# Kernel optimization log

Measured on AMD Instinct MI355X. Metric: run time of the kernel, lower is better.

## Reference

```python
import jax, jax.numpy as jnp
import numpy as np

B, T = 64, 64
HUMAN, IN = 64, 8
HS, ES, K = 1024, 1024, 7
PSI_H, PSI_LR = 1024, 30

_PAR_SHAPES = [(HS, HS), (HS,), (IN, HS), (HS, HUMAN), (IN, HUMAN - IN)]
_PAR_SIZES = [int(np.prod(s)) for s in _PAR_SHAPES]
N_PSI = int(sum(_PAR_SIZES))
_OFFS = np.cumsum([0] + _PAR_SIZES)


def setup_inputs() -> dict:
    key = jax.random.key(0)
    ks = jax.random.split(key, 16)
    def xav(k, shape):
        lim = float(np.sqrt(6.0 / (shape[0] + shape[1])))
        return jax.random.uniform(k, shape, minval=-lim, maxval=lim, dtype=jnp.float32)
    def uni(k, shape, s):
        return jax.random.uniform(k, shape, minval=-s, maxval=s, dtype=jnp.float32)
    se = float(1.0 / np.sqrt(ES))
    return {
        "inputs": jax.random.normal(ks[0], (B, T, IN), jnp.float32),
        "outputs": jax.random.normal(ks[1], (B, T, HUMAN), jnp.float32),
        "eps": jax.random.normal(ks[2], (B, K), jnp.float32),
        "enc_Wih": uni(ks[3], (3 * ES, HUMAN), se),
        "enc_Whh": uni(ks[4], (3 * ES, ES), se),
        "enc_bih": uni(ks[5], (3 * ES,), se),
        "enc_bhh": uni(ks[6], (3 * ES,), se),
        "to_mu": xav(ks[7], (ES, K)),
        "to_lsigma": xav(ks[8], (ES, K)),
        "to_lsigma_bias": -0.5 * jnp.ones((K,), jnp.float32),
        "W1": xav(ks[9], (K, PSI_H)),
        "b1": jnp.zeros((PSI_H,), jnp.float32),
        "W2": xav(ks[10], (PSI_H, PSI_LR)),
        "b2": jnp.zeros((PSI_LR,), jnp.float32),
        "W3": xav(ks[11], (PSI_LR, N_PSI)),
        "b3": jnp.zeros((N_PSI,), jnp.float32),
        "gru_Wih": xav(ks[12], (IN, 2 * HS)),
        "gru_Whh": xav(ks[13], (HS, 2 * HS)),
        "gru_bias": jnp.concatenate([jnp.zeros((HS,)), jnp.ones((HS,))]).astype(jnp.float32),
    }


def _gru_cell(h, x, Wih, Whh, bih, bhh):
    # torch.nn.GRUCell math, gate order (r, z, n)
    gx = x @ Wih.T + bih
    gh = h @ Whh.T + bhh
    xr, xz, xn = jnp.split(gx, 3, axis=-1)
    hr, hz, hn = jnp.split(gh, 3, axis=-1)
    r = jax.nn.sigmoid(xr + hr)
    z = jax.nn.sigmoid(xz + hz)
    n = jnp.tanh(xn + r * hn)
    return (1.0 - z) * n + z * h


def _split_psi(psi):
    # psi: [B, N_PSI] -> per-sample (Whh, bh, Wih, C, D)
    return [psi[:, _OFFS[i]:_OFFS[i + 1]].reshape((-1,) + _PAR_SHAPES[i]) for i in range(5)]


def reference(inputs, outputs, eps, enc_Wih, enc_Whh, enc_bih, enc_bhh,
              to_mu, to_lsigma, to_lsigma_bias, W1, b1, W2, b2, W3, b3,
              gru_Wih, gru_Whh, gru_bias):
    bsz = inputs.shape[0]
    # ---- encoder: GRUCell over time-major outputs ----
    out_tm = jnp.swapaxes(outputs, 0, 1)  # [T, B, HUMAN]
    h0 = jnp.zeros((bsz, ES), inputs.dtype)
    h_enc = _gru_cell(h0, out_tm[0], enc_Wih, enc_Whh, enc_bih, enc_bhh)
    def enc_step(h, x):
        h = _gru_cell(h, x, enc_Wih, enc_Whh, enc_bih, enc_bhh)
        return h, None
    h_enc, _ = jax.lax.scan(enc_step, h_enc, out_tm[1:])
    mu = h_enc @ to_mu                       # [B, K]
    logstd = h_enc @ to_lsigma + to_lsigma_bias
    z = mu + eps * jnp.exp(logstd)
    # ---- hypernetwork psi decoder ----
    psi = (jnp.tanh(z @ W1 + b1) @ W2 + b2) @ W3 + b3   # [B, N_PSI]
    Whh_b, bh_b, Wih_b, C_b, D_b = _split_psi(psi)
    # ---- per-sample GRU decoder, vectorized over batch, scan over time ----
    gx_all = jnp.einsum('bti,ij->tbj', inputs, gru_Wih)  # [T, B, 2*HS]
    xW_all = jnp.einsum('bti,bih->tbh', inputs, Wih_b)   # [T, B, HS]

    def dec_step(h, xs):
        gx_t, xW_t = xs
        pre = gx_t + h @ gru_Whh + gru_bias   # [B, 2*HS]
        z_t = jax.nn.sigmoid(pre[:, :HS])
        r_t = jax.nn.sigmoid(pre[:, HS:])
        hWhh = jnp.einsum('bh,bhk->bk', h, Whh_b) + bh_b
        eta = jnp.tanh(xW_t + r_t * jnp.tanh(hWhh))
        h_new = z_t * h + (1.0 - z_t) * eta
        return h_new, h_new

    state0 = jnp.zeros((bsz, HS), inputs.dtype)
    h_last, dec_seq = jax.lax.scan(dec_step, state0, (gx_all, xW_all))
    dec_seq = jnp.swapaxes(dec_seq, 0, 1)    # [B, T, HS]
    # ---- readout ----
    yhats = jnp.einsum('bth,bhm->btm', dec_seq, C_b)
    xD = jnp.einsum('bti,bim->btm', inputs, D_b)  # [B, T, HUMAN-IN]
    yhats = yhats + jnp.concatenate([jnp.zeros_like(inputs), xD], axis=-1)
    # residual output
    yhats = yhats + jnp.concatenate(
        [inputs, jnp.zeros((bsz, inputs.shape[1], HUMAN - IN), inputs.dtype)], axis=-1)
    states = jax.lax.stop_gradient(h_last)
    return yhats, mu, logstd, states
```

## Files before the change

### kernel.cpp

```cpp
#include <hip/hip_runtime.h>

namespace {
constexpr int nT = 64;
constexpr int nK = 7;
constexpr long N_PSI = 1123776;
constexpr long SZ_WHH = 1048576;
constexpr long REST_SZ = 75200;
constexpr long R_BH = 0;
constexpr long R_WIH = 1024;
constexpr long R_C = 9216;
constexpr long R_D = 74752;
constexpr int NCH = 16;
constexpr long PHALF = (long)NCH * 64 * 1024;
}

typedef __attribute__((ext_vector_type(4))) unsigned short us4;

__device__ __forceinline__ float b2f(unsigned short u) {
  return __uint_as_float(((unsigned int)u) << 16);
}
__device__ __forceinline__ unsigned short f2b(float f) {
  unsigned int u = __float_as_uint(f);
  return (unsigned short)((u + 0x7fffu + ((u >> 16) & 1u)) >> 16);
}
__device__ __forceinline__ float sigm(float x) { return 1.f / (1.f + __expf(-x)); }

__global__ void transpose_bf16_k(const float* __restrict__ in, unsigned short* __restrict__ out,
                                 int rows, int cols) {
  __shared__ float tile[32][33];
  int x = blockIdx.x * 32 + threadIdx.x;
  int y = blockIdx.y * 32 + threadIdx.y;
  #pragma unroll
  for (int i = 0; i < 32; i += 8)
    if ((y + i) < rows && x < cols) tile[threadIdx.y + i][threadIdx.x] = in[(long)(y + i) * cols + x];
  __syncthreads();
  x = blockIdx.y * 32 + threadIdx.x;
  y = blockIdx.x * 32 + threadIdx.y;
  #pragma unroll
  for (int i = 0; i < 32; i += 8)
    if ((y + i) < cols && x < rows) out[(long)(y + i) * rows + x] = f2b(tile[threadIdx.x][threadIdx.y + i]);
}

__global__ void cvt_bf16_k(const float* __restrict__ in, unsigned short* __restrict__ out, long n) {
  long i = (long)blockIdx.x * 256 + threadIdx.x;
  if (i < n) out[i] = f2b(in[i]);
}

__global__ __launch_bounds__(256) void enc_gx_k(const float* __restrict__ outputs,
                                                const unsigned short* __restrict__ WtWihB,
                                                const float* __restrict__ bih,
                                                unsigned short* __restrict__ gxE) {
  int g0 = blockIdx.x * 256;
  int btg = blockIdx.y;
  __shared__ unsigned short ws[64 * 256];
  __shared__ float xs[64][64];
  for (int i = threadIdx.x; i < 64 * 256; i += 256)
    ws[i] = WtWihB[(long)(i >> 8) * 3072 + g0 + (i & 255)];
  for (int i = threadIdx.x; i < 64 * 64; i += 256) {
    int idx = btg * 64 + (i >> 6);
    int t = idx >> 6, b = idx & 63;
    xs[i >> 6][i & 63] = outputs[((long)b * nT + t) * 64 + (i & 63)];
  }
  __syncthreads();
  float bihv = bih[g0 + threadIdx.x];
  for (int j = 0; j < 64; ++j) {
    int idx = btg * 64 + j;
    float acc = bihv;
    #pragma unroll 8
    for (int i = 0; i < 64; ++i) acc += xs[j][i] * b2f(ws[i * 256 + threadIdx.x]);
    gxE[(long)idx * 3072 + g0 + threadIdx.x] = f2b(acc);
  }
}

__global__ __launch_bounds__(256) void dec_gx_k(const float* __restrict__ inputs,
                                                const float* __restrict__ gWih,
                                                const float* __restrict__ gbias,
                                                unsigned short* __restrict__ gxD) {
  int g0 = blockIdx.x * 256;
  int btg = blockIdx.y;
  __shared__ float ws[8][256];
  __shared__ float xs[64][8];
  for (int i = threadIdx.x; i < 8 * 256; i += 256)
    ws[i >> 8][i & 255] = gWih[(long)(i >> 8) * 2048 + g0 + (i & 255)];
  for (int i = threadIdx.x; i < 64 * 8; i += 256) {
    int idx = btg * 64 + (i >> 3);
    int t = idx >> 6, b = idx & 63;
    xs[i >> 3][i & 7] = inputs[((long)b * nT + t) * 8 + (i & 7)];
  }
  __syncthreads();
  float bv = gbias[g0 + threadIdx.x];
  for (int j = 0; j < 64; ++j) {
    int idx = btg * 64 + j;
    float acc = bv;
    #pragma unroll
    for (int i = 0; i < 8; ++i) acc += xs[j][i] * ws[i][threadIdx.x];
    gxD[(long)idx * 2048 + g0 + threadIdx.x] = f2b(acc);
  }
}

__global__ __launch_bounds__(256) void xW_k(const float* __restrict__ inputs,
                                            const float* __restrict__ Rest,
                                            unsigned short* __restrict__ xWb) {
  int k0 = blockIdx.x * 256;
  int b = blockIdx.y;
  __shared__ float ws[8][256];
  __shared__ float xs[64][8];
  const float* RB = Rest + (long)b * REST_SZ + R_WIH;
  for (int i = threadIdx.x; i < 8 * 256; i += 256)
    ws[i >> 8][i & 255] = RB[(long)(i >> 8) * 1024 + k0 + (i & 255)];
  for (int i = threadIdx.x; i < 64 * 8; i += 256)
    xs[i >> 3][i & 7] = inputs[((long)b * nT + (i >> 3)) * 8 + (i & 7)];
  __syncthreads();
  for (int t = 0; t < 64; ++t) {
    float acc = 0.f;
    #pragma unroll
    for (int i = 0; i < 8; ++i) acc += xs[t][i] * ws[i][threadIdx.x];
    xWb[((long)t * 64 + b) * 1024 + k0 + threadIdx.x] = f2b(acc);
  }
}

__global__ __launch_bounds__(512, 2) void enc_step3_k(
    const unsigned short* __restrict__ W,
    const unsigned short* __restrict__ gxE,
    const float* __restrict__ bhh,
    float* __restrict__ hEnc,
    const float* __restrict__ pRr, const float* __restrict__ pZr, const float* __restrict__ pNr,
    float* __restrict__ pRw, float* __restrict__ pZw, float* __restrict__ pNw,
    int t) {
  int c = blockIdx.x & (NCH - 1);
  int sp = blockIdx.x >> 4;
  int b0 = sp * 2, b1 = b0 + 1;
  __shared__ float h0s[64], h1s[64];
  __shared__ float red[3][4][128];
  int v = threadIdx.x;
  {
    int q = v >> 7, idx = v & 127;
    int bb = (idx >> 6) ? b1 : b0;
    int e = c * 64 + (idx & 63);
    float sr = 0.f, sz = 0.f, sn = 0.f;
    if (t > 0) {
      #pragma unroll
      for (int cc = q * 4; cc < q * 4 + 4; ++cc) {
        long base = ((long)cc * 64 + bb) * 1024 + e;
        sr += pRr[base]; sz += pZr[base]; sn += pNr[base];
      }
    }
    red[0][q][idx] = sr; red[1][q][idx] = sz; red[2][q][idx] = sn;
  }
  __syncthreads();
  if (v < 128) {
    int hi = v >> 6;
    int bb = hi ? b1 : b0;
    int e = c * 64 + (v & 63);
    float sr = red[0][0][v] + red[0][1][v] + red[0][2][v] + red[0][3][v];
    float sz = red[1][0][v] + red[1][1][v] + red[1][2][v] + red[1][3][v];
    float sn = red[2][0][v] + red[2][1][v] + red[2][2][v] + red[2][3][v];
    long gb = ((long)t * 64 + bb) * 3072;
    float xr = b2f(gxE[gb + e]), xz = b2f(gxE[gb + 1024 + e]), xn = b2f(gxE[gb + 2048 + e]);
    float hr = sr + bhh[e], hz = sz + bhh[1024 + e], hn = sn + bhh[2048 + e];
    float r = sigm(xr + hr);
    float z = sigm(xz + hz);
    float n = tanhf(xn + r * hn);
    float hold = (t > 0) ? hEnc[(long)bb * 1024 + e] : 0.f;
    float hnew = (1.f - z) * n + z * hold;
    hEnc[(long)bb * 1024 + e] = hnew;
    if (hi) h1s[v & 63] = hnew; else h0s[v & 63] = hnew;
  }
  __syncthreads();
  if (t < nT - 1) {
    if (v < 256) {
      int e0 = v * 4;
      float ar0[4] = {}, az0[4] = {}, ar1[4] = {}, az1[4] = {};
      const unsigned short* Wb = W + (long)(c * 64) * 3072 + e0;
      #pragma unroll 4
      for (int j = 0; j < 64; ++j) {
        us4 wr = *(const us4*)(Wb + (long)j * 3072);
        us4 wz = *(const us4*)(Wb + (long)j * 3072 + 1024);
        float hv0 = h0s[j], hv1 = h1s[j];
        #pragma unroll
        for (int q = 0; q < 4; ++q) {
          float fr = b2f(wr[q]), fz = b2f(wz[q]);
          ar0[q] += hv0 * fr; az0[q] += hv0 * fz;
          ar1[q] += hv1 * fr; az1[q] += hv1 * fz;
        }
      }
      long i0 = ((long)c * 64 + b0) * 1024 + e0;
      long i1 = i0 + 1024;
      *(float4*)(pRw + i0) = make_float4(ar0[0], ar0[1], ar0[2], ar0[3]);
      *(float4*)(pZw + i0) = make_float4(az0[0], az0[1], az0[2], az0[3]);
      *(float4*)(pRw + i1) = make_float4(ar1[0], ar1[1], ar1[2], ar1[3]);
      *(float4*)(pZw + i1) = make_float4(az1[0], az1[1], az1[2], az1[3]);
    } else {
      int e0 = (v - 256) * 4;
      float an0[4] = {}, an1[4] = {};
      const unsigned short* Wb = W + (long)(c * 64) * 3072 + 2048 + e0;
      #pragma unroll 8
      for (int j = 0; j < 64; ++j) {
        us4 wn = *(const us4*)(Wb + (long)j * 3072);
        float hv0 = h0s[j], hv1 = h1s[j];
        #pragma unroll
        for (int q = 0; q < 4; ++q) {
          float fn = b2f(wn[q]);
          an0[q] += hv0 * fn; an1[q] += hv1 * fn;
        }
      }
      long i0 = ((long)c * 64 + b0) * 1024 + e0;
      long i1 = i0 + 1024;
      *(float4*)(pNw + i0) = make_float4(an0[0], an0[1], an0[2], an0[3]);
      *(float4*)(pNw + i1) = make_float4(an1[0], an1[1], an1[2], an1[3]);
    }
  }
}

__global__ __launch_bounds__(256) void latent_hyper_k(
    const float* __restrict__ h_enc,
    const float* __restrict__ to_mu, const float* __restrict__ to_lsig,
    const float* __restrict__ lsig_bias, const float* __restrict__ eps,
    const float* __restrict__ W1, const float* __restrict__ b1,
    const float* __restrict__ W2, const float* __restrict__ b2,
    float* __restrict__ out_mu, float* __restrict__ out_lsig,
    float* __restrict__ a2out) {
  int b = blockIdx.x;
  __shared__ float hs[1024];
  __shared__ float zv[8];
  __shared__ float a1[1024];
  for (int i = threadIdx.x; i < 1024; i += 256) hs[i] = h_enc[b * 1024 + i];
  __syncthreads();
  int g = threadIdx.x >> 5, s = threadIdx.x & 31;
  if (g < nK) {
    float am = 0.f, as_ = 0.f;
    for (int h = s; h < 1024; h += 32) {
      float hv = hs[h];
      am += hv * to_mu[h * nK + g];
      as_ += hv * to_lsig[h * nK + g];
    }
    #pragma unroll
    for (int m = 16; m >= 1; m >>= 1) { am += __shfl_xor(am, m); as_ += __shfl_xor(as_, m); }
    if (s == 0) {
      float ls = as_ + lsig_bias[g];
      out_mu[b * nK + g] = am;
      out_lsig[b * nK + g] = ls;
      zv[g] = am + eps[b * nK + g] * __expf(ls);
    }
  }
  __syncthreads();
  for (int j = threadIdx.x; j < 1024; j += 256) {
    float acc = b1[j];
    #pragma unroll
    for (int i = 0; i < nK; ++i) acc += zv[i] * W1[i * 1024 + j];
    a1[j] = tanhf(acc);
  }
  __syncthreads();
  int l = threadIdx.x >> 3, s8 = threadIdx.x & 7;
  if (l < 30) {
    float acc = 0.f;
    for (int j = s8; j < 1024; j += 8) acc += a1[j] * W2[j * 30 + l];
    acc += __shfl_xor(acc, 4);
    acc += __shfl_xor(acc, 2);
    acc += __shfl_xor(acc, 1);
    if (s8 == 0) a2out[b * 30 + l] = acc + b2[l];
  }
}

__global__ __launch_bounds__(256) void psi_q8_k(
    const float* __restrict__ a2, const float* __restrict__ W3, const float* __restrict__ b3,
    char* __restrict__ Q8, float* __restrict__ sdec ) {
  __shared__ float sa[64 * 30];
  for (int i = threadIdx.x; i < 64 * 30; i += 256) sa[i] = a2[i];
  int h = blockIdx.x >> 1, half = blockIdx.x & 1;
  int wv = threadIdx.x >> 6, lane = threadIdx.x & 63;
  int g = half * 4 + wv;
  long n0 = (long)h * 1024 + g * 128 + lane * 2;
  float2 w[30];
  #pragma unroll
  for (int l = 0; l < 30; ++l) w[l] = *(const float2*)(W3 + (long)l * N_PSI + n0);
  float2 bb = *(const float2*)(b3 + n0);
  __syncthreads();
  for (int b = 0; b < 64; ++b) {
    float a0 = bb.x, a1 = bb.y;
    const float* ab = &sa[b * 30];
    #pragma unroll
    for (int l = 0; l < 30; ++l) { float av = ab[l]; a0 += av * w[l].x; a1 += av * w[l].y; }
    float m = fmaxf(fabsf(a0), fabsf(a1));
    #pragma unroll
    for (int d = 32; d >= 1; d >>= 1) m = fmaxf(m, __shfl_xor(m, d));
    float inv = (m > 0.f) ? 127.f / m : 0.f;
    int q0 = __float2int_rn(a0 * inv);
    int q1 = __float2int_rn(a1 * inv);
    q0 = min(127, max(-127, q0));
    q1 = min(127, max(-127, q1));
    *(char2*)(Q8 + (long)b * SZ_WHH + n0) = make_char2((char)q0, (char)q1);
    if (lane == 0) sdec[((long)b * 1024 + h) * 8 + g] = m * (1.f / 127.f);
  }
}

__global__ __launch_bounds__(256) void psi_rest_k(
    const float* __restrict__ a2, const float* __restrict__ W3, const float* __restrict__ b3,
    float* __restrict__ Rest) {
  __shared__ float sa[64 * 30];
  for (int i = threadIdx.x; i < 64 * 30; i += 256) sa[i] = a2[i];
  long n0 = SZ_WHH + ((long)blockIdx.x * 256 + threadIdx.x) * 2;
  __syncthreads();
  if (n0 >= N_PSI) return;
  float2 w[30];
  #pragma unroll
  for (int l = 0; l < 30; ++l) w[l] = *(const float2*)(W3 + (long)l * N_PSI + n0);
  float2 bb = *(const float2*)(b3 + n0);
  long r = n0 - SZ_WHH;
  for (int b = 0; b < 64; ++b) {
    float a0 = bb.x, a1 = bb.y;
    const float* ab = &sa[b * 30];
    #pragma unroll
    for (int l = 0; l < 30; ++l) { float av = ab[l]; a0 += av * w[l].x; a1 += av * w[l].y; }
    *(float2*)(Rest + (long)b * REST_SZ + r) = make_float2(a0, a1);
  }
}

__global__ __launch_bounds__(512, 2) void dec_step_q8g_k(
    const char* __restrict__ Q8,
    const float* __restrict__ sdec,
    const unsigned short* __restrict__ gWhhB,
    const unsigned short* __restrict__ gxD,
    const unsigned short* __restrict__ xWb,
    const float* __restrict__ Rest,
    float* __restrict__ decS,
    const float* __restrict__ pZr, const float* __restrict__ pRr, const float* __restrict__ pWr,
    float* __restrict__ pZw, float* __restrict__ pRw, float* __restrict__ pWw,
    int t) {
  int c = blockIdx.x & (NCH - 1);
  int sp = blockIdx.x >> 4;
  int b0 = sp * 2, b1 = b0 + 1;
  __shared__ float h0s[64], h1s[64];
  __shared__ float h0q[8][64], h1q[8][64];
  __shared__ float red[3][4][128];
  int v = threadIdx.x;
  {
    int q = v >> 7, idx = v & 127;
    int bb = (idx >> 6) ? b1 : b0;
    int k = c * 64 + (idx & 63);
    float sz = 0.f, sr = 0.f, sw = 0.f;
    if (t > 0) {
      #pragma unroll
      for (int cc = q * 4; cc < q * 4 + 4; ++cc) {
        long base = ((long)cc * 64 + bb) * 1024 + k;
        sz += pZr[base]; sr += pRr[base]; sw += pWr[base];
      }
    }
    red[0][q][idx] = sz; red[1][q][idx] = sr; red[2][q][idx] = sw;
  }
  __syncthreads();
  if (v < 128) {
    int hi = v >> 6;
    int bb = hi ? b1 : b0;
    int k = c * 64 + (v & 63);
    float sz = red[0][0][v] + red[0][1][v] + red[0][2][v] + red[0][3][v];
    float sr = red[1][0][v] + red[1][1][v] + red[1][2][v] + red[1][3][v];
    float sw = red[2][0][v] + red[2][1][v] + red[2][2][v] + red[2][3][v];
    long gb = ((long)t * 64 + bb) * 2048;
    float gz = b2f(gxD[gb + k]), gr = b2f(gxD[gb + 1024 + k]);
    float z = sigm(gz + sz);
    float r = sigm(gr + sr);
    float hW = sw + Rest[(long)bb * REST_SZ + R_BH + k];
    float xw = b2f(xWb[((long)t * 64 + bb) * 1024 + k]);
    float eta = tanhf(xw + r * tanhf(hW));
    float hold = (t > 0) ? decS[((long)bb * nT + (t - 1)) * 1024 + k] : 0.f;
    float hnew = z * hold + (1.f - z) * eta;
    decS[((long)bb * nT + t) * 1024 + k] = hnew;
    const float* sc = sdec + ((long)bb * 1024 + k) * 8;
    float4 scA = *(const float4*)(sc);
    float4 scB = *(const float4*)(sc + 4);
    int row = v & 63;
    if (hi) {
      h1s[row] = hnew;
      h1q[0][row] = hnew * scA.x; h1q[1][row] = hnew * scA.y;
      h1q[2][row] = hnew * scA.z; h1q[3][row] = hnew * scA.w;
      h1q[4][row] = hnew * scB.x; h1q[5][row] = hnew * scB.y;
      h1q[6][row] = hnew * scB.z; h1q[7][row] = hnew * scB.w;
    } else {
      h0s[row] = hnew;
      h0q[0][row] = hnew * scA.x; h0q[1][row] = hnew * scA.y;
      h0q[2][row] = hnew * scA.z; h0q[3][row] = hnew * scA.w;
      h0q[4][row] = hnew * scB.x; h0q[5][row] = hnew * scB.y;
      h0q[6][row] = hnew * scB.z; h0q[7][row] = hnew * scB.w;
    }
  }
  __syncthreads();
  if (t < nT - 1) {
    if (v < 256) {
      int k0 = v * 4;
      float az0[4] = {}, ar0[4] = {}, az1[4] = {}, ar1[4] = {};
      const unsigned short* G = gWhhB + (long)(c * 64) * 2048 + k0;
      #pragma unroll 4
      for (int j = 0; j < 64; ++j) {
        us4 wz = *(const us4*)(G + (long)j * 2048);
        us4 wr = *(const us4*)(G + (long)j * 2048 + 1024);
        float hv0 = h0s[j], hv1 = h1s[j];
        #pragma unroll
        for (int q = 0; q < 4; ++q) {
          float fz = b2f(wz[q]), fr = b2f(wr[q]);
          az0[q] += hv0 * fz; ar0[q] += hv0 * fr;
          az1[q] += hv1 * fz; ar1[q] += hv1 * fr;
        }
      }
      long i0 = ((long)c * 64 + b0) * 1024 + k0;
      long i1 = i0 + 1024;
      *(float4*)(pZw + i0) = make_float4(az0[0], az0[1], az0[2], az0[3]);
      *(float4*)(pRw + i0) = make_float4(ar0[0], ar0[1], ar0[2], ar0[3]);
      *(float4*)(pZw + i1) = make_float4(az1[0], az1[1], az1[2], az1[3]);
      *(float4*)(pRw + i1) = make_float4(ar1[0], ar1[1], ar1[2], ar1[3]);
    } else {
      int k0 = (v - 256) * 4;
      int g = k0 >> 7;
      const float* hq0 = h0q[g];
      const float* hq1 = h1q[g];
      float aw0[4] = {}, aw1[4] = {};
      const char* Q0 = Q8 + (long)b0 * SZ_WHH + (long)(c * 64) * 1024 + k0;
      const char* Q1 = Q8 + (long)b1 * SZ_WHH + (long)(c * 64) * 1024 + k0;
      #pragma unroll 8
      for (int j = 0; j < 64; ++j) {
        char4 q0 = *(const char4*)(Q0 + (long)j * 1024);
        char4 q1 = *(const char4*)(Q1 + (long)j * 1024);
        float hv0 = hq0[j], hv1 = hq1[j];
        aw0[0] += hv0 * (float)q0.x; aw0[1] += hv0 * (float)q0.y;
        aw0[2] += hv0 * (float)q0.z; aw0[3] += hv0 * (float)q0.w;
        aw1[0] += hv1 * (float)q1.x; aw1[1] += hv1 * (float)q1.y;
        aw1[2] += hv1 * (float)q1.z; aw1[3] += hv1 * (float)q1.w;
      }
      long i0 = ((long)c * 64 + b0) * 1024 + k0;
      long i1 = i0 + 1024;
      *(float4*)(pWw + i0) = make_float4(aw0[0], aw0[1], aw0[2], aw0[3]);
      *(float4*)(pWw + i1) = make_float4(aw1[0], aw1[1], aw1[2], aw1[3]);
    }
  }
}

__global__ __launch_bounds__(256) void readout_k(
    const float* __restrict__ dec_seq, const float* __restrict__ inputs,
    const float* __restrict__ Rest, float* __restrict__ yhats) {
  int b = blockIdx.x >> 3;
  int tg = blockIdx.x & 7;
  __shared__ float ss[8][1024];
  __shared__ float part[4][8][64];
  for (int i = threadIdx.x; i < 8 * 1024; i += 256)
    ss[i >> 10][i & 1023] = dec_seq[((long)b * nT + tg * 8 + (i >> 10)) * 1024 + (i & 1023)];
  __syncthreads();
  int m = threadIdx.x & 63, hq = threadIdx.x >> 6;
  const float* C = Rest + (long)b * REST_SZ + R_C;
  float acc[8] = {};
  for (int h = hq * 256; h < hq * 256 + 256; ++h) {
    float cv = C[(long)h * 64 + m];
    #pragma unroll
    for (int tt = 0; tt < 8; ++tt) acc[tt] += ss[tt][h] * cv;
  }
  #pragma unroll
  for (int tt = 0; tt < 8; ++tt) part[hq][tt][m] = acc[tt];
  __syncthreads();
  const float* D = Rest + (long)b * REST_SZ + R_D;
  for (int o = threadIdx.x; o < 512; o += 256) {
    int tt = o >> 6, mm = o & 63;
    float a = part[0][tt][mm] + part[1][tt][mm] + part[2][tt][mm] + part[3][tt][mm];
    long bt = (long)b * nT + tg * 8 + tt;
    if (mm < 8) {
      a += inputs[bt * 8 + mm];
    } else {
      #pragma unroll
      for (int i = 0; i < 8; ++i) a += inputs[bt * 8 + i] * D[i * 56 + (mm - 8)];
    }
    yhats[bt * 64 + mm] = a;
  }
}

__global__ void copy_states_k(const float* __restrict__ dec_seq, float* __restrict__ states) {
  int i = blockIdx.x * 256 + threadIdx.x;
  int b = i >> 10, h = i & 1023;
  states[i] = dec_seq[((long)b * nT + (nT - 1)) * 1024 + h];
}

extern "C" void kernel_launch(void* const* d_in, const int* in_sizes, int n_in,
                              void* d_out, int out_size, void* d_ws, size_t ws_size,
                              hipStream_t stream) {
  const float* inputs  = (const float*)d_in[0];
  const float* outputs = (const float*)d_in[1];
  const float* eps     = (const float*)d_in[2];
  const float* enc_Wih = (const float*)d_in[3];
  const float* enc_Whh = (const float*)d_in[4];
  const float* enc_bih = (const float*)d_in[5];
  const float* enc_bhh = (const float*)d_in[6];
  const float* to_mu   = (const float*)d_in[7];
  const float* to_lsig = (const float*)d_in[8];
  const float* lsig_b  = (const float*)d_in[9];
  const float* W1 = (const float*)d_in[10];
  const float* b1 = (const float*)d_in[11];
  const float* W2 = (const float*)d_in[12];
  const float* b2 = (const float*)d_in[13];
  const float* W3 = (const float*)d_in[14];
  const float* b3 = (const float*)d_in[15];
  const float* gWih  = (const float*)d_in[16];
  const float* gWhh  = (const float*)d_in[17];
  const float* gbias = (const float*)d_in[18];

  char* ws = (char*)d_ws;
  size_t off = 0;
  auto alloc = [&](size_t bytes) { size_t o = off; off = (off + bytes + 255) & ~(size_t)255; return o; };
  size_t oRest   = alloc(64ull * REST_SZ * 4);
  size_t oQ8     = alloc(64ull * SZ_WHH);
  size_t oSdec   = alloc(64ull * 1024 * 8 * 4);
  size_t ogWhhB  = alloc(1024ull * 2048 * 2);
  size_t oWtWhhB = alloc(1024ull * 3072 * 2);
  size_t oWtWihB = alloc(64ull * 3072 * 2);
  size_t ogxE    = alloc(64ull * 64 * 3072 * 2);
  size_t ogxD    = alloc(64ull * 64 * 2048 * 2);
  size_t oxWb    = alloc(64ull * 64 * 1024 * 2);
  size_t opA     = alloc((size_t)2 * PHALF * 4);
  size_t opB     = alloc((size_t)2 * PHALF * 4);
  size_t opC     = alloc((size_t)2 * PHALF * 4);
  size_t ohA     = alloc(64ull * 1024 * 4);
  size_t oDec    = alloc(64ull * 64 * 1024 * 4);
  size_t oA2     = alloc(64 * 30 * 4);
  (void)in_sizes; (void)n_in; (void)out_size; (void)ws_size;

  float*          Rest   = (float*)(ws + oRest);
  char*           Q8     = (char*)(ws + oQ8);
  float*          sdec   = (float*)(ws + oSdec);
  unsigned short* gWhhB  = (unsigned short*)(ws + ogWhhB);
  unsigned short* WtWhhB = (unsigned short*)(ws + oWtWhhB);
  unsigned short* WtWihB = (unsigned short*)(ws + oWtWihB);
  unsigned short* gxE    = (unsigned short*)(ws + ogxE);
  unsigned short* gxD    = (unsigned short*)(ws + ogxD);
  unsigned short* xWb    = (unsigned short*)(ws + oxWb);
  float* pA   = (float*)(ws + opA);
  float* pB   = (float*)(ws + opB);
  float* pC   = (float*)(ws + opC);
  float* hA   = (float*)(ws + ohA);
  float* decS = (float*)(ws + oDec);
  float* a2   = (float*)(ws + oA2);

  float* out    = (float*)d_out;
  float* out_yh = out;
  float* out_mu = out + 262144;
  float* out_ls = out + 262144 + 448;
  float* out_st = out + 262144 + 896;

  transpose_bf16_k<<<dim3(32, 96), dim3(32, 8), 0, stream>>>(enc_Whh, WtWhhB, 3072, 1024);
  transpose_bf16_k<<<dim3(2, 96),  dim3(32, 8), 0, stream>>>(enc_Wih, WtWihB, 3072, 64);
  cvt_bf16_k<<<(int)((1024ull * 2048 + 255) / 256), 256, 0, stream>>>(gWhh, gWhhB, 1024 * 2048);

  enc_gx_k<<<dim3(12, 64), 256, 0, stream>>>(outputs, WtWihB, enc_bih, gxE);

  for (int t = 0; t < nT; ++t) {
    int rp = t & 1, wp = (t + 1) & 1;
    enc_step3_k<<<512, 512, 0, stream>>>(WtWhhB, gxE, enc_bhh, hA,
        pA + (size_t)rp * PHALF, pB + (size_t)rp * PHALF, pC + (size_t)rp * PHALF,
        pA + (size_t)wp * PHALF, pB + (size_t)wp * PHALF, pC + (size_t)wp * PHALF, t);
  }

  latent_hyper_k<<<64, 256, 0, stream>>>(hA, to_mu, to_lsig, lsig_b, eps,
                                         W1, b1, W2, b2, out_mu, out_ls, a2);
  psi_q8_k<<<2048, 256, 0, stream>>>(a2, W3, b3, Q8, sdec);
  psi_rest_k<<<(int)((REST_SZ / 2 + 255) / 256), 256, 0, stream>>>(a2, W3, b3, Rest);

  dec_gx_k<<<dim3(8, 64), 256, 0, stream>>>(inputs, gWih, gbias, gxD);
  xW_k<<<dim3(4, 64), 256, 0, stream>>>(inputs, Rest, xWb);

  for (int t = 0; t < nT; ++t) {
    int rp = t & 1, wp = (t + 1) & 1;
    dec_step_q8g_k<<<512, 512, 0, stream>>>(Q8, sdec, gWhhB, gxD, xWb, Rest, decS,
        pA + (size_t)rp * PHALF, pB + (size_t)rp * PHALF, pC + (size_t)rp * PHALF,
        pA + (size_t)wp * PHALF, pB + (size_t)wp * PHALF, pC + (size_t)wp * PHALF, t);
  }

  readout_k<<<512, 256, 0, stream>>>(decS, inputs, Rest, out_yh);
  copy_states_k<<<256, 256, 0, stream>>>(decS, out_st);
}
```

Before: 2.755 ms.

## Change int8 psi quantization grouping to share scales across four samples

```diff
diff --git a/kernel.cpp b/kernel.cpp
--- a/kernel.cpp
+++ b/kernel.cpp
@@ -267,30 +267,37 @@
     char* __restrict__ Q8, float* __restrict__ sdec ) {
   __shared__ float sa[64 * 30];
   for (int i = threadIdx.x; i < 64 * 30; i += 256) sa[i] = a2[i];
-  int h = blockIdx.x >> 1, half = blockIdx.x & 1;
+  int h = blockIdx.x >> 2, q4 = blockIdx.x & 3;
   int wv = threadIdx.x >> 6, lane = threadIdx.x & 63;
-  int g = half * 4 + wv;
-  long n0 = (long)h * 1024 + g * 128 + lane * 2;
-  float2 w[30];
+  int g = q4 * 4 + wv;
+  long n0 = (long)h * 1024 + q4 * 256 + threadIdx.x;
+  float w[30];
   #pragma unroll
-  for (int l = 0; l < 30; ++l) w[l] = *(const float2*)(W3 + (long)l * N_PSI + n0);
-  float2 bb = *(const float2*)(b3 + n0);
-  __syncthreads();
-  for (int b = 0; b < 64; ++b) {
-    float a0 = bb.x, a1 = bb.y;
-    const float* ab = &sa[b * 30];
-    #pragma unroll
-    for (int l = 0; l < 30; ++l) { float av = ab[l]; a0 += av * w[l].x; a1 += av * w[l].y; }
-    float m = fmaxf(fabsf(a0), fabsf(a1));
+  for (int l = 0; l < 30; ++l) w[l] = W3[(long)l * N_PSI + n0];
+  float bb = b3[n0];
+  __syncthreads();
+  for (int bq = 0; bq < 16; ++bq) {
+    float vv[4];
+    #pragma unroll
+    for (int s = 0; s < 4; ++s) {
+      int b = bq * 4 + s;
+      float a0 = bb;
+      const float* ab = &sa[b * 30];
+      #pragma unroll
+      for (int l = 0; l < 30; ++l) a0 += ab[l] * w[l];
+      vv[s] = a0;
+    }
+    float m = fmaxf(fmaxf(fabsf(vv[0]), fabsf(vv[1])), fmaxf(fabsf(vv[2]), fabsf(vv[3])));
     #pragma unroll
     for (int d = 32; d >= 1; d >>= 1) m = fmaxf(m, __shfl_xor(m, d));
     float inv = (m > 0.f) ? 127.f / m : 0.f;
-    int q0 = __float2int_rn(a0 * inv);
-    int q1 = __float2int_rn(a1 * inv);
-    q0 = min(127, max(-127, q0));
-    q1 = min(127, max(-127, q1));
-    *(char2*)(Q8 + (long)b * SZ_WHH + n0) = make_char2((char)q0, (char)q1);
-    if (lane == 0) sdec[((long)b * 1024 + h) * 8 + g] = m * (1.f / 127.f);
+    #pragma unroll
+    for (int s = 0; s < 4; ++s) {
+      int q = __float2int_rn(vv[s] * inv);
+      q = min(127, max(-127, q));
+      Q8[(long)(bq * 4 + s) * SZ_WHH + n0] = (char)q;
+    }
+    if (lane == 0) sdec[((long)bq * 1024 + h) * 16 + g] = m * (1.f / 127.f);
   }
 }
 
@@ -316,7 +323,7 @@
   }
 }
 
-__global__ __launch_bounds__(512, 2) void dec_step_q8g_k(
+__global__ __launch_bounds__(512, 2) void dec_step_q8h_k(
     const char* __restrict__ Q8,
     const float* __restrict__ sdec,
     const unsigned short* __restrict__ gWhhB,
@@ -331,7 +338,7 @@
   int sp = blockIdx.x >> 4;
   int b0 = sp * 2, b1 = b0 + 1;
   __shared__ float h0s[64], h1s[64];
-  __shared__ float h0q[8][64], h1q[8][64];
+  __shared__ float h0q[16][68], h1q[16][68];
   __shared__ float red[3][4][128];
   int v = threadIdx.x;
   {
@@ -366,22 +373,17 @@
     float hold = (t > 0) ? decS[((long)bb * nT + (t - 1)) * 1024 + k] : 0.f;
     float hnew = z * hold + (1.f - z) * eta;
     decS[((long)bb * nT + t) * 1024 + k] = hnew;
-    const float* sc = sdec + ((long)bb * 1024 + k) * 8;
-    float4 scA = *(const float4*)(sc);
-    float4 scB = *(const float4*)(sc + 4);
+    const float* sc = sdec + ((long)(bb >> 2) * 1024 + k) * 16;
     int row = v & 63;
-    if (hi) {
-      h1s[row] = hnew;
-      h1q[0][row] = hnew * scA.x; h1q[1][row] = hnew * scA.y;
-      h1q[2][row] = hnew * scA.z; h1q[3][row] = hnew * scA.w;
-      h1q[4][row] = hnew * scB.x; h1q[5][row] = hnew * scB.y;
-      h1q[6][row] = hnew * scB.z; h1q[7][row] = hnew * scB.w;
-    } else {
-      h0s[row] = hnew;
-      h0q[0][row] = hnew * scA.x; h0q[1][row] = hnew * scA.y;
-      h0q[2][row] = hnew * scA.z; h0q[3][row] = hnew * scA.w;
-      h0q[4][row] = hnew * scB.x; h0q[5][row] = hnew * scB.y;
-      h0q[6][row] = hnew * scB.z; h0q[7][row] = hnew * scB.w;
+    float (*hq)[68] = hi ? h1q : h0q;
+    if (hi) h1s[row] = hnew; else h0s[row] = hnew;
+    #pragma unroll
+    for (int gg = 0; gg < 16; gg += 4) {
+      float4 s4 = *(const float4*)(sc + gg);
+      hq[gg + 0][row] = hnew * s4.x;
+      hq[gg + 1][row] = hnew * s4.y;
+      hq[gg + 2][row] = hnew * s4.z;
+      hq[gg + 3][row] = hnew * s4.w;
     }
   }
   __syncthreads();
@@ -410,7 +412,7 @@
       *(float4*)(pRw + i1) = make_float4(ar1[0], ar1[1], ar1[2], ar1[3]);
     } else {
       int k0 = (v - 256) * 4;
-      int g = k0 >> 7;
+      int g = k0 >> 6;
       const float* hq0 = h0q[g];
       const float* hq1 = h1q[g];
       float aw0[4] = {}, aw1[4] = {};
@@ -436,7 +438,8 @@
 
 __global__ __launch_bounds__(256) void readout_k(
     const float* __restrict__ dec_seq, const float* __restrict__ inputs,
-    const float* __restrict__ Rest, float* __restrict__ yhats) {
+    const float* __restrict__ Rest, float* __restrict__ yhats,
+    float* __restrict__ states) {
   int b = blockIdx.x >> 3;
   int tg = blockIdx.x & 7;
   __shared__ float ss[8][1024];
@@ -444,6 +447,10 @@
   for (int i = threadIdx.x; i < 8 * 1024; i += 256)
     ss[i >> 10][i & 1023] = dec_seq[((long)b * nT + tg * 8 + (i >> 10)) * 1024 + (i & 1023)];
   __syncthreads();
+  if (tg == 7) {
+    for (int i = threadIdx.x; i < 1024; i += 256)
+      states[(long)b * 1024 + i] = ss[7][i];
+  }
   int m = threadIdx.x & 63, hq = threadIdx.x >> 6;
   const float* C = Rest + (long)b * REST_SZ + R_C;
   float acc[8] = {};
@@ -468,12 +475,6 @@
     }
     yhats[bt * 64 + mm] = a;
   }
-}
-
-__global__ void copy_states_k(const float* __restrict__ dec_seq, float* __restrict__ states) {
-  int i = blockIdx.x * 256 + threadIdx.x;
-  int b = i >> 10, h = i & 1023;
-  states[i] = dec_seq[((long)b * nT + (nT - 1)) * 1024 + h];
 }
 
 extern "C" void kernel_launch(void* const* d_in, const int* in_sizes, int n_in,
@@ -504,7 +505,7 @@
   auto alloc = [&](size_t bytes) { size_t o = off; off = (off + bytes + 255) & ~(size_t)255; return o; };
   size_t oRest   = alloc(64ull * REST_SZ * 4);
   size_t oQ8     = alloc(64ull * SZ_WHH);
-  size_t oSdec   = alloc(64ull * 1024 * 8 * 4);
+  size_t oSdec   = alloc(16ull * 1024 * 16 * 4);
   size_t ogWhhB  = alloc(1024ull * 2048 * 2);
   size_t oWtWhhB = alloc(1024ull * 3072 * 2);
   size_t oWtWihB = alloc(64ull * 3072 * 2);
@@ -556,7 +557,7 @@
 
   latent_hyper_k<<<64, 256, 0, stream>>>(hA, to_mu, to_lsig, lsig_b, eps,
                                          W1, b1, W2, b2, out_mu, out_ls, a2);
-  psi_q8_k<<<2048, 256, 0, stream>>>(a2, W3, b3, Q8, sdec);
+  psi_q8_k<<<4096, 256, 0, stream>>>(a2, W3, b3, Q8, sdec);
   psi_rest_k<<<(int)((REST_SZ / 2 + 255) / 256), 256, 0, stream>>>(a2, W3, b3, Rest);
 
   dec_gx_k<<<dim3(8, 64), 256, 0, stream>>>(inputs, gWih, gbias, gxD);
@@ -564,11 +565,10 @@
 
   for (int t = 0; t < nT; ++t) {
     int rp = t & 1, wp = (t + 1) & 1;
-    dec_step_q8g_k<<<512, 512, 0, stream>>>(Q8, sdec, gWhhB, gxD, xWb, Rest, decS,
+    dec_step_q8h_k<<<512, 512, 0, stream>>>(Q8, sdec, gWhhB, gxD, xWb, Rest, decS,
         pA + (size_t)rp * PHALF, pB + (size_t)rp * PHALF, pC + (size_t)rp * PHALF,
         pA + (size_t)wp * PHALF, pB + (size_t)wp * PHALF, pC + (size_t)wp * PHALF, t);
   }
 
-  readout_k<<<512, 256, 0, stream>>>(decS, inputs, Rest, out_yh);
-  copy_states_k<<<256, 256, 0, stream>>>(decS, out_st);
-}
+  readout_k<<<512, 256, 0, stream>>>(decS, inputs, Rest, out_yh, out_st);
+}
```

New measurement: 2.748 ms, median of 2. About the same (-0.2%).
